# Optimization experiments

Measured on AMD Instinct MI355X. Metric: run time of the kernel, lower is better.

The kernel has to match this reference:

```python
import jax, jax.numpy as jnp
import numpy as np

B, C, H, W = 4, 64, 64, 64  # x shape; mask is (B,1,8H,8W)


def _conv(x, w, pad=0):
    return jax.lax.conv_general_dilated(
        x, w, (1, 1), [(pad, pad), (pad, pad)],
        dimension_numbers=('NCHW', 'OIHW', 'NCHW'))


def _inorm(x, eps=1e-5):  # InstanceNorm2d, affine=False, biased var (torch default)
    mu = x.mean(axis=(2, 3), keepdims=True)
    var = x.var(axis=(2, 3), keepdims=True)
    return (x - mu) * jax.lax.rsqrt(var + eps)


def _forward(x, mask, kconv_w1, kconv_w2, fs_w1, fs_w2, fs_b2, fs_fuse_w):
    b, c, h, w = x.shape
    n = h * w
    # MaxPool2d(8,8) then binarize
    m = jax.lax.reduce_window(mask, -jnp.inf, jax.lax.max,
                              (1, 1, 8, 8), (1, 1, 8, 8), 'VALID')
    m = (m > 0).astype(x.dtype)
    back = 1.0 - m
    # ResidualBlock K_conv (shared for K and Q paths in original code)
    y = jax.nn.relu(_inorm(_conv(x, kconv_w1, pad=1)))
    y = _inorm(_conv(y, kconv_w2, pad=1))
    kx = jax.nn.relu(y + x)
    # L2-normalized K/Q over channel dim
    K = (kx * back).reshape(b, c, n)
    K = K / (jnp.linalg.norm(K, axis=1, keepdims=True) + 1e-8)
    Q = (kx * m).reshape(b, c, n)
    Q = Q / (jnp.linalg.norm(Q, axis=1, keepdims=True) + 1e-8)
    V = (x * back).reshape(b, c, n)
    # cosine-similarity score map, temperature 20
    score = jnp.einsum('bcq,bck->bqk', Q, K) * 20.0  # (b, n_q, n_k)
    qm = m.reshape(b, 1, n)      # query mask (foreground)
    km = back.reshape(b, 1, n)   # key mask (background)
    NEG = -1000000.0
    validx = score + (1.0 - km) * NEG + (1.0 - qm.transpose(0, 2, 1)) * NEG
    att = jax.nn.softmax(validx, axis=-1) * (qm.transpose(0, 2, 1) * km)
    # att_fore[b,c,q] = sum_k V[b,c,k] * att[b,q,k]
    att_fore = jnp.einsum('bck,bqk->bcq', V, att).reshape(b, c, h, w)
    # Fusion_score
    feat1 = _conv(jnp.concatenate([x * m, att_fore * m], axis=1), fs_w1)
    s = jax.nn.sigmoid(_conv(feat1, fs_w2) + fs_b2[None, :, None, None])
    fused = _conv(jnp.concatenate([x * m, att_fore * m * (1.0 - s)], axis=1), fs_fuse_w)
    fs_out = fused * m + x * (1.0 - m)
    out = fs_out * m + x * (1.0 - m)
    # visualization attention mask
    visatt = att.sum(axis=1).reshape(b, 1, h, w)
    attmask = jnp.repeat(jnp.repeat(visatt, 8, axis=2), 8, axis=3)  # nearest upsample x8
    attmask = attmask / attmask.max()
    return out, attmask


def setup_inputs() -> dict:
    key = jax.random.key(0)
    ks = jax.random.split(key, 8)

    def wgt(k, shape, fan_in):
        return jax.random.normal(k, shape, jnp.float32) / np.sqrt(fan_in)

    x = jax.random.normal(ks[0], (B, C, H, W), jnp.float32)
    # sparse foreground mask so maxpool(8x8)>0 yields a mixed fg/bg mask
    mask = (jax.random.uniform(ks[1], (B, 1, H * 8, W * 8)) < 0.01).astype(jnp.float32)
    return dict(
        x=x, mask=mask,
        kconv_w1=wgt(ks[2], (C, C, 3, 3), C * 9),
        kconv_w2=wgt(ks[3], (C, C, 3, 3), C * 9),
        fs_w1=wgt(ks[4], (C, 2 * C, 1, 1), 2 * C),
        fs_w2=wgt(ks[5], (C, C, 1, 1), C),
        fs_b2=jnp.zeros((C,), jnp.float32),
        fs_fuse_w=wgt(ks[6], (C, 2 * C, 1, 1), 2 * C),
    )


def reference(x, mask, kconv_w1, kconv_w2, fs_w1, fs_w2, fs_b2, fs_fuse_w):
    return _forward(x, mask, kconv_w1, kconv_w2, fs_w1, fs_w2, fs_b2, fs_fuse_w)
```

## Files before the change

### kernel.cpp

```cpp
#include <hip/hip_runtime.h>
#include <hip/hip_bf16.h>

typedef __hip_bfloat16 bf16;
typedef __attribute__((ext_vector_type(8))) short short8;
typedef __attribute__((ext_vector_type(4))) float f32x4;
typedef __attribute__((ext_vector_type(16))) float f32x16;

#define BB 4
#define CC 64
#define NN 4096
#define MH 512
#define MW 512
#define LS 72
#define NPARTS 16
#define NDEN 16

#define WB_Y1T  ((size_t)0)
#define WB_VIS  ((size_t)4259840)
#define WB_QIX  ((size_t)4325376)
#define WB_KIX  ((size_t)4390912)
#define WB_MFL  ((size_t)4456448)
#define WB_CNT  ((size_t)4472832)
#define WB_WT1  ((size_t)4476992)
#define WB_WT2  ((size_t)4550720)
#define WB_WFB  ((size_t)4624448)
#define WB_KC   ((size_t)5242880)
#define WB_XT   ((size_t)8388608)
#define WB_KXT  ((size_t)10485760)
#define WB_VT   ((size_t)12582912)
#define WB_QC   ((size_t)14680064)
#define WB_E    ((size_t)16777216)
#define EB_ELEM ((size_t)16777216)
#define WB_AFCP ((size_t)150994944)
#define WB_DENP ((size_t)218103808)
#define WB_VISP ((size_t)220200960)
#define WB_GST  ((size_t)220725248)

__device__ __forceinline__ float us2f(unsigned short u) { return __uint_as_float(((unsigned)u) << 16); }
__device__ __forceinline__ unsigned short f2bu(float f) {
  bf16 h = __float2bfloat16(f);
  return *(unsigned short*)&h;
}

__global__ __launch_bounds__(256) void k_pre(const float* __restrict__ x,
                                             const float* __restrict__ mask,
                                             const float* __restrict__ w1,
                                             const float* __restrict__ w2,
                                             const float* __restrict__ fw1,
                                             const float* __restrict__ fw2,
                                             const float* __restrict__ fwf,
                                             float* __restrict__ outp,
                                             unsigned short* __restrict__ xt,
                                             unsigned char* __restrict__ mfl,
                                             float* __restrict__ vis,
                                             unsigned int* __restrict__ vmaxb,
                                             unsigned short* __restrict__ wT1,
                                             unsigned short* __restrict__ wT2,
                                             unsigned short* __restrict__ wfb) {
  __shared__ float lx[64][65];
  int t = threadIdx.x;
  if (blockIdx.x < 256) {
    int b = blockIdx.x >> 6, p0 = (blockIdx.x & 63) * 64;
    const float* xb = x + (size_t)b * CC * NN + p0;
    float* ob = outp + (size_t)b * CC * NN + p0;
    for (int idx = t; idx < 4096; idx += 256) {
      int c = idx >> 6, j = idx & 63;
      float v = xb[c * NN + j];
      lx[j][c] = v;
      ob[c * NN + j] = v;
    }
    __syncthreads();
    unsigned short* xo = xt + ((size_t)b * NN + p0) * 64;
    for (int idx = t; idx < 2048; idx += 256) {
      int j = idx >> 5, c2 = (idx & 31) * 2;
      ushort2 w2v;
      w2v.x = f2bu(lx[j][c2]);
      w2v.y = f2bu(lx[j][c2 + 1]);
      *(ushort2*)&xo[j * 64 + c2] = w2v;
    }
  } else {
    int g = (blockIdx.x - 256) * 256 + t;
    int o = g >> 2, sub = g & 3;
    int b = o >> 12, p = o & 4095;
    int py = p >> 6, px = p & 63;
    const float* mb = mask + (size_t)b * MH * MW + (py * 8 + sub * 2) * MW + px * 8;
    float mx = 0.f;
    #pragma unroll
    for (int dy = 0; dy < 2; ++dy) {
      const float4* r4 = (const float4*)(mb + dy * MW);
      float4 a = r4[0], c = r4[1];
      mx = fmaxf(mx, fmaxf(fmaxf(a.x, a.y), fmaxf(a.z, a.w)));
      mx = fmaxf(mx, fmaxf(fmaxf(c.x, c.y), fmaxf(c.z, c.w)));
    }
    mx = fmaxf(mx, __shfl_xor(mx, 1));
    mx = fmaxf(mx, __shfl_xor(mx, 2));
    if (sub == 0) {
      mfl[o] = (mx > 0.f) ? 1 : 0;
      vis[o] = 0.f;
    }
    if (g == 0) vmaxb[0] = 0u;
    if (g < 36864) {
      int tap = g >> 12;
      int rem = g & 4095;
      int co = rem >> 6, ci = rem & 63;
      int src = (co * 64 + ci) * 9 + tap;
      wT1[g] = f2bu(w1[src]);
      wT2[g] = f2bu(w2[src]);
    } else if (g < 57344) {
      int j2 = g - 36864;
      if (j2 < 8192)       wfb[j2] = f2bu(fw1[j2]);
      else if (j2 < 12288) wfb[j2] = f2bu(fw2[j2 - 8192]);
      else                 wfb[j2] = f2bu(fwf[j2 - 12288]);
    }
  }
}

__global__ __launch_bounds__(256) void k_compact(const unsigned char* __restrict__ mfl,
                                                 int* __restrict__ qidx, int* __restrict__ kidx,
                                                 int* __restrict__ nq, int* __restrict__ nk) {
  int b = blockIdx.x;
  __shared__ unsigned char lm[4096];
  int t = threadIdx.x;
  *(uint4*)&lm[t * 16] = *(const uint4*)&mfl[b * NN + t * 16];
  __syncthreads();
  if (t >= 64) return;
  int lane = t;
  int qb = 0, kb = 0;
  #pragma unroll
  for (int it = 0; it < 64; ++it) {
    int p = it * 64 + lane;
    bool f = lm[p] != 0;
    unsigned long long bal = __ballot(f);
    int before = __popcll(bal & ((1ULL << lane) - 1ULL));
    if (f)  qidx[b * NN + qb + before] = p;
    if (!f) kidx[b * NN + kb + (lane - before)] = p;
    int cnt = __popcll(bal);
    qb += cnt; kb += 64 - cnt;
  }
  if (lane == 0) { nq[b] = qb; nk[b] = kb; }
}

template <bool NORM_IN>
__global__ __launch_bounds__(256) void k_convm(const unsigned short* __restrict__ src,
                                               const unsigned short* __restrict__ wT,
                                               const float* __restrict__ insum,
                                               const float* __restrict__ insq,
                                               unsigned short* __restrict__ dst,
                                               float* __restrict__ gsump,
                                               float* __restrict__ gsqp) {
  int b = blockIdx.y;
  int r = blockIdx.x;
  __shared__ unsigned short bx[198 * LS];
  __shared__ float nmean[64], ninv[64];
  int t = threadIdx.x;
  if (NORM_IN) {
    if (t < 64) {
      float s = 0.f, s2v = 0.f;
      #pragma unroll 8
      for (int r2 = 0; r2 < 64; ++r2) {
        s   += insum[((size_t)r2 * BB + b) * 64 + t];
        s2v += insq [((size_t)r2 * BB + b) * 64 + t];
      }
      float m = s * (1.f / NN);
      float v = fmaxf(s2v * (1.f / NN) - m * m, 0.f);
      nmean[t] = m; ninv[t] = rsqrtf(v + 1e-5f);
    }
    __syncthreads();
  }
  const unsigned short* sb = src + (size_t)b * NN * 64;
  for (int idx = t; idx < 198 * 8; idx += 256) {
    int row = idx >> 3, c8 = (idx & 7) * 8;
    int dy = row / 66;
    int cx = row - dy * 66 - 1;
    int rr = r + dy - 1;
    uint4 v = make_uint4(0u, 0u, 0u, 0u);
    if ((unsigned)rr < 64u && (unsigned)cx < 64u) {
      v = *(const uint4*)(sb + ((size_t)(rr * 64 + cx)) * 64 + c8);
      if (NORM_IN) {
        unsigned short* e = (unsigned short*)&v;
        #pragma unroll
        for (int j = 0; j < 8; ++j)
          e[j] = f2bu(fmaxf((us2f(e[j]) - nmean[c8 + j]) * ninv[c8 + j], 0.f));
      }
    }
    *(uint4*)&bx[row * LS + c8] = v;
  }
  __syncthreads();
  int lane = t & 63;
  int quad = lane >> 4, col = lane & 15;
  int qw = (t >> 6) * 16;
  f32x4 acc[4] = {{0.f,0.f,0.f,0.f},{0.f,0.f,0.f,0.f},{0.f,0.f,0.f,0.f},{0.f,0.f,0.f,0.f}};
  #pragma unroll
  for (int tap = 0; tap < 9; ++tap) {
    int dy = tap / 3, dx = tap - dy * 3 - 1;
    const unsigned short* wrow = wT + ((size_t)tap * 64 + qw + col) * 64;
    short8 a0 = *(const short8*)(wrow + quad * 8);
    short8 a1 = *(const short8*)(wrow + 32 + quad * 8);
    int rbase = dy * 66 + dx + 1;
    #pragma unroll
    for (int nt = 0; nt < 4; ++nt) {
      int row = rbase + nt * 16 + col;
      short8 b0 = *(const short8*)&bx[row * LS + quad * 8];
      short8 b1 = *(const short8*)&bx[row * LS + 32 + quad * 8];
      acc[nt] = __builtin_amdgcn_mfma_f32_16x16x32_bf16(a0, b0, acc[nt], 0, 0, 0);
      acc[nt] = __builtin_amdgcn_mfma_f32_16x16x32_bf16(a1, b1, acc[nt], 0, 0, 0);
    }
  }
  #pragma unroll
  for (int rr = 0; rr < 4; ++rr) {
    float s1 = acc[0][rr] + acc[1][rr] + acc[2][rr] + acc[3][rr];
    float s2 = acc[0][rr]*acc[0][rr] + acc[1][rr]*acc[1][rr]
             + acc[2][rr]*acc[2][rr] + acc[3][rr]*acc[3][rr];
    s1 += __shfl_xor(s1, 1); s2 += __shfl_xor(s2, 1);
    s1 += __shfl_xor(s1, 2); s2 += __shfl_xor(s2, 2);
    s1 += __shfl_xor(s1, 4); s2 += __shfl_xor(s2, 4);
    s1 += __shfl_xor(s1, 8); s2 += __shfl_xor(s2, 8);
    if (col == 0) {
      int co = qw + quad * 4 + rr;
      gsump[((size_t)r * BB + b) * 64 + co] = s1;
      gsqp [((size_t)r * BB + b) * 64 + co] = s2;
    }
  }
  __syncthreads();
  #pragma unroll
  for (int nt = 0; nt < 4; ++nt)
    #pragma unroll
    for (int rr = 0; rr < 4; ++rr)
      bx[(nt * 16 + col) * LS + qw + quad * 4 + rr] = f2bu(acc[nt][rr]);
  __syncthreads();
  unsigned short* db = dst + ((size_t)b * NN + r * 64) * 64;
  for (int idx = t; idx < 512; idx += 256) {
    int px = idx >> 3, c8 = (idx & 7) * 8;
    *(uint4*)(db + (size_t)px * 64 + c8) = *(const uint4*)&bx[px * LS + c8];
  }
}

__global__ __launch_bounds__(256) void k_gath(const unsigned short* __restrict__ kxt,
                                              const unsigned short* __restrict__ xt,
                                              const int* __restrict__ qidx, const int* __restrict__ kidx,
                                              const int* __restrict__ nqv, const int* __restrict__ nkv,
                                              const float* __restrict__ gsump,
                                              const float* __restrict__ gsqp,
                                              unsigned short* __restrict__ kc,
                                              unsigned short* __restrict__ vt,
                                              unsigned short* __restrict__ qc) {
  int b = blockIdx.y;
  int j0 = blockIdx.x * 64;
  int nqb = nqv[b], nkb = nkv[b];
  int NKP = (nkb + 63) & ~63, NQP = (nqb + 63) & ~63;
  bool dok = j0 < NKP, doq = j0 < NQP;
  if (!dok && !doq) return;
  __shared__ int li[128];
  __shared__ unsigned short tv[64 * LS];
  __shared__ float m2[64], i2[64];
  int t = threadIdx.x;
  if (t < 64) li[t] = (j0 + t < nkb) ? kidx[b * NN + j0 + t] : -1;
  if (t >= 64 && t < 128) li[t] = (j0 + (t - 64) < nqb) ? qidx[b * NN + j0 + (t - 64)] : -1;
  if (t >= 128 && t < 192) {
    int c = t - 128;
    float s = 0.f, s2v = 0.f;
    #pragma unroll 8
    for (int r2 = 0; r2 < 64; ++r2) {
      s   += gsump[((size_t)r2 * BB + b) * 64 + c];
      s2v += gsqp [((size_t)r2 * BB + b) * 64 + c];
    }
    float m = s * (1.f / NN);
    float v = fmaxf(s2v * (1.f / NN) - m * m, 0.f);
    m2[c] = m; i2[c] = rsqrtf(v + 1e-5f);
  }
  __syncthreads();
  const unsigned short* kxb = kxt + (size_t)b * NN * 64;
  const unsigned short* xtb = xt + (size_t)b * NN * 64;
  uint4 z = make_uint4(0u, 0u, 0u, 0u);
  for (int idx = t; idx < 512; idx += 256) {
    int row = idx >> 3, c8 = (idx & 7) * 8;
    size_t dsto = ((size_t)b * NN + j0 + row) * 64 + c8;
    if (dok) {
      int sk = li[row];
      uint4 ko = z;
      if (sk >= 0) {
        uint4 kv = *(const uint4*)(kxb + (size_t)sk * 64 + c8);
        uint4 xv = *(const uint4*)(xtb + (size_t)sk * 64 + c8);
        const unsigned short* ke = (const unsigned short*)&kv;
        const unsigned short* xe = (const unsigned short*)&xv;
        float f[8]; float ss = 0.f;
        #pragma unroll
        for (int j = 0; j < 8; ++j) {
          float v = fmaxf((us2f(ke[j]) - m2[c8 + j]) * i2[c8 + j] + us2f(xe[j]), 0.f);
          f[j] = v; ss += v * v;
        }
        ss += __shfl_xor(ss, 1); ss += __shfl_xor(ss, 2); ss += __shfl_xor(ss, 4);
        float inv = 1.f / (sqrtf(ss) + 1e-8f);
        unsigned short* oe = (unsigned short*)&ko;
        #pragma unroll
        for (int j = 0; j < 8; ++j) oe[j] = f2bu(f[j] * inv);
        *(uint4*)&tv[row * LS + c8] = xv;
      } else {
        float ss = 0.f;
        ss += __shfl_xor(ss, 1); ss += __shfl_xor(ss, 2); ss += __shfl_xor(ss, 4);
        *(uint4*)&tv[row * LS + c8] = z;
      }
      *(uint4*)(kc + dsto) = ko;
    }
    if (doq) {
      int sq = li[64 + row];
      uint4 qo = z;
      if (sq >= 0) {
        uint4 kv = *(const uint4*)(kxb + (size_t)sq * 64 + c8);
        uint4 xv = *(const uint4*)(xtb + (size_t)sq * 64 + c8);
        const unsigned short* ke = (const unsigned short*)&kv;
        const unsigned short* xe = (const unsigned short*)&xv;
        float f[8]; float ss = 0.f;
        #pragma unroll
        for (int j = 0; j < 8; ++j) {
          float v = fmaxf((us2f(ke[j]) - m2[c8 + j]) * i2[c8 + j] + us2f(xe[j]), 0.f);
          f[j] = v; ss += v * v;
        }
        ss += __shfl_xor(ss, 1); ss += __shfl_xor(ss, 2); ss += __shfl_xor(ss, 4);
        float inv = 1.f / (sqrtf(ss) + 1e-8f);
        unsigned short* oe = (unsigned short*)&qo;
        #pragma unroll
        for (int j = 0; j < 8; ++j) oe[j] = f2bu(f[j] * inv);
      } else {
        float ss = 0.f;
        ss += __shfl_xor(ss, 1); ss += __shfl_xor(ss, 2); ss += __shfl_xor(ss, 4);
      }
      *(uint4*)(qc + dsto) = qo;
    }
  }
  __syncthreads();
  if (!dok) return;
  for (int idx = t; idx < 512; idx += 256) {
    int c = idx >> 3, k8 = (idx & 7) * 8;
    unsigned short vals[8];
    #pragma unroll
    for (int j = 0; j < 8; ++j) vals[j] = tv[(k8 + j) * LS + c];
    *(uint4*)(vt + (size_t)b * 262144 + (size_t)c * 4096 + j0 + k8) = *(const uint4*)&vals[0];
  }
}

__global__ __launch_bounds__(256) void k_att1(const unsigned short* __restrict__ kc,
                                              const unsigned short* __restrict__ vt,
                                              const unsigned short* __restrict__ qc,
                                              const int* __restrict__ nqv, const int* __restrict__ nkv,
                                              unsigned short* __restrict__ afc_part,
                                              float* __restrict__ den_part,
                                              unsigned short* __restrict__ eg) {
  __shared__ unsigned short leb[4][32 * LS];
  int b = blockIdx.y;
  int nqb = nqv[b], nkb = nkv[b];
  int t = threadIdx.x;
  int wave = t >> 6, lane = t & 63;
  int part = blockIdx.x & (NPARTS - 1);
  int q0 = ((blockIdx.x >> 4) * 4 + wave) * 32;
  if (q0 >= nqb) return;
  int ntiles = (nkb + 63) >> 6;
  int nt_blk = (part < ntiles) ? ((ntiles - part + NPARTS - 1) >> 4) : 0;
  int NKP = (nkb + 63) & ~63;
  unsigned short* le = leb[wave];
  int l31 = lane & 31, lhi = lane >> 5;
  const unsigned short* kcb = kc + (size_t)b * NN * 64;
  const unsigned short* vtb = vt + (size_t)b * 262144;
  const unsigned short* qcb = qc + (size_t)b * NN * 64;
  unsigned short* egb = eg + (size_t)b * EB_ELEM;
  unsigned short* afcp = afc_part + ((size_t)b * NN) * (NPARTS * 64);
  float* denp = den_part + ((size_t)b * NN) * NDEN;
  short8 aq[4];
  #pragma unroll
  for (int ks = 0; ks < 4; ++ks)
    aq[ks] = *(const short8*)(qcb + (size_t)(q0 + l31) * 64 + ks * 16 + lhi * 8);
  f32x16 pv0, pv1, dsum;
  #pragma unroll
  for (int i = 0; i < 16; ++i) { pv0[i] = 0.f; pv1[i] = 0.f; dsum[i] = 0.f; }
  for (int it = 0; it < nt_blk; ++it) {
    int j0 = (part + it * NPARTS) * 64;
    #pragma unroll
    for (int kh = 0; kh < 2; ++kh) {
      f32x16 s;
      #pragma unroll
      for (int i = 0; i < 16; ++i) s[i] = 0.f;
      const unsigned short* krow = kcb + (size_t)(j0 + kh * 32 + l31) * 64 + lhi * 8;
      #pragma unroll
      for (int ks = 0; ks < 4; ++ks) {
        short8 bk = *(const short8*)(krow + ks * 16);
        s = __builtin_amdgcn_mfma_f32_32x32x16_bf16(aq[ks], bk, s, 0, 0, 0);
      }
      bool kval = (j0 + kh * 32 + l31) < nkb;
      #pragma unroll
      for (int reg = 0; reg < 16; ++reg) {
        float e = kval ? __expf(20.f * s[reg]) : 0.f;
        dsum[reg] += e;
        int row = (reg & 3) + 8 * (reg >> 2) + 4 * lhi;
        le[row * LS + kh * 32 + l31] = f2bu(e);
      }
    }
    #pragma unroll
    for (int ks = 0; ks < 4; ++ks) {
      short8 a = *(const short8*)&le[l31 * LS + ks * 16 + lhi * 8];
      short8 bv0 = *(const short8*)(vtb + (size_t)l31 * 4096 + j0 + ks * 16 + lhi * 8);
      short8 bv1 = *(const short8*)(vtb + (size_t)(32 + l31) * 4096 + j0 + ks * 16 + lhi * 8);
      pv0 = __builtin_amdgcn_mfma_f32_32x32x16_bf16(a, bv0, pv0, 0, 0, 0);
      pv1 = __builtin_amdgcn_mfma_f32_32x32x16_bf16(a, bv1, pv1, 0, 0, 0);
    }
    #pragma unroll
    for (int sub = 0; sub < 4; ++sub) {
      int idx = sub * 64 + lane;
      int q = idx >> 3, cc8 = (idx & 7) * 8;
      if (q0 + q < nqb)
        *(uint4*)(egb + (size_t)(q0 + q) * NKP + j0 + cc8) = *(const uint4*)&le[q * LS + cc8];
    }
  }
  #pragma unroll
  for (int reg = 0; reg < 16; ++reg) {
    float v = dsum[reg];
    v += __shfl_xor(v, 1); v += __shfl_xor(v, 2); v += __shfl_xor(v, 4);
    v += __shfl_xor(v, 8); v += __shfl_xor(v, 16);
    int row = (reg & 3) + 8 * (reg >> 2) + 4 * lhi;
    int qq = q0 + row;
    if (l31 == 0 && qq < nqb) denp[(size_t)qq * NDEN + part] = v;
  }
  #pragma unroll
  for (int reg = 0; reg < 16; ++reg) {
    int row = (reg & 3) + 8 * (reg >> 2) + 4 * lhi;
    int qq = q0 + row;
    if (qq < nqb) {
      unsigned short* ap = afcp + ((size_t)qq * NPARTS + part) * 64;
      ap[l31]      = f2bu(pv0[reg]);
      ap[32 + l31] = f2bu(pv1[reg]);
    }
  }
}

__global__ __launch_bounds__(256) void k_vis(const unsigned short* __restrict__ eg,
                                             const float* __restrict__ den_part,
                                             const int* __restrict__ nqv, const int* __restrict__ nkv,
                                             float* __restrict__ visp) {
  int b = blockIdx.z;
  int nqb = nqv[b], nkb = nkv[b];
  int k0 = blockIdx.x * 256;
  if (k0 >= nkb) return;
  int NKP = (nkb + 63) & ~63;
  int qpart = blockIdx.y;
  int qbeg = (qpart * nqb) >> 3;
  int qend = ((qpart + 1) * nqb) >> 3;
  __shared__ float wd[256];
  int t = threadIdx.x;
  int k = k0 + t;
  const unsigned short* eb = eg + (size_t)b * EB_ELEM;
  float acc = 0.f;
  for (int qc = qbeg; qc < qend; qc += 256) {
    __syncthreads();
    int qq = qc + t;
    float d = 0.f;
    if (qq < qend) {
      const float4* dp = (const float4*)(den_part + ((size_t)b * NN + qq) * NDEN);
      float4 a0 = dp[0], a1 = dp[1], a2 = dp[2], a3 = dp[3];
      d = ((a0.x + a0.y) + (a0.z + a0.w)) + ((a1.x + a1.y) + (a1.z + a1.w))
        + ((a2.x + a2.y) + (a2.z + a2.w)) + ((a3.x + a3.y) + (a3.z + a3.w));
    }
    wd[t] = (d > 0.f) ? 1.f / d : 0.f;
    __syncthreads();
    int lim = min(256, qend - qc);
    if (k < nkb) {
      const unsigned short* ep = eb + (size_t)qc * NKP + k;
      int j = 0;
      for (; j + 8 <= lim; j += 8) {
        #pragma unroll
        for (int u = 0; u < 8; ++u)
          acc += us2f(ep[(size_t)(j + u) * NKP]) * wd[j + u];
      }
      for (; j < lim; ++j)
        acc += us2f(ep[(size_t)j * NKP]) * wd[j];
    }
  }
  if (k < nkb) visp[((size_t)qpart * BB + b) * NN + k] = acc;
}

#define FS 136
__global__ __launch_bounds__(256) void k_fusionm(const unsigned short* __restrict__ xt,
                                                 const unsigned short* __restrict__ afc_part,
                                                 const float* __restrict__ den_part,
                                                 const int* __restrict__ qidx, const int* __restrict__ nqv,
                                                 const unsigned short* __restrict__ wall,
                                                 const float* __restrict__ b2,
                                                 float* __restrict__ outp) {
  int b = blockIdx.y;
  int nqb = nqv[b];
  int q0 = blockIdx.x * 64;
  if (q0 >= nqb) return;
  __shared__ unsigned short pxa[64 * FS];
  __shared__ unsigned short f1s[64 * LS];
  __shared__ int qpl[64];
  int t = threadIdx.x;
  int lane = t & 63;
  int quad = lane >> 4, col = lane & 15;
  int cb = (t >> 6) * 16;
  const int* qix = qidx + b * NN;
  const unsigned short* xtb = xt + (size_t)b * NN * 64;
  const unsigned short* w1b = wall;
  const unsigned short* w2b = wall + 8192;
  const unsigned short* wfb = wall + 12288;
  short8 a1[4], a2[2], af[4];
  #pragma unroll
  for (int kt = 0; kt < 4; ++kt) {
    a1[kt] = *(const short8*)&w1b[(cb + col) * 128 + kt * 32 + quad * 8];
    af[kt] = *(const short8*)&wfb[(cb + col) * 128 + kt * 32 + quad * 8];
  }
  #pragma unroll
  for (int kt = 0; kt < 2; ++kt)
    a2[kt] = *(const short8*)&w2b[(cb + col) * 64 + kt * 32 + quad * 8];
  float b2v[4];
  #pragma unroll
  for (int r = 0; r < 4; ++r) b2v[r] = b2[cb + quad * 4 + r];
  if (t < 64) qpl[t] = (q0 + t < nqb) ? qix[q0 + t] : -1;
  for (int idx = t; idx < 512; idx += 256) {
    int q = idx >> 3, c8 = (idx & 7) * 8;
    int qq = q0 + q;
    uint4 pv = make_uint4(0u, 0u, 0u, 0u);
    unsigned short pa8[8] = {0, 0, 0, 0, 0, 0, 0, 0};
    if (qq < nqb) {
      int qp = qix[qq];
      pv = *(const uint4*)(xtb + (size_t)qp * 64 + c8);
      const float* db = den_part + ((size_t)b * NN + qq) * NDEN;
      float d = 0.f;
      #pragma unroll
      for (int p2 = 0; p2 < NDEN; ++p2) d += db[p2];
      float av[8];
      #pragma unroll
      for (int j = 0; j < 8; ++j) av[j] = 0.f;
      const unsigned short* ab = afc_part + ((size_t)b * NN + qq) * (NPARTS * 64) + c8;
      #pragma unroll
      for (int p2 = 0; p2 < NPARTS; ++p2) {
        const uint4 u = *(const uint4*)(ab + p2 * 64);
        const unsigned short* e8 = (const unsigned short*)&u;
        #pragma unroll
        for (int j = 0; j < 8; ++j) av[j] += us2f(e8[j]);
      }
      float invd = (d > 0.f) ? 1.f / d : 0.f;
      #pragma unroll
      for (int j = 0; j < 8; ++j) pa8[j] = f2bu(av[j] * invd);
    }
    *(uint4*)&pxa[q * FS + c8] = pv;
    *(uint4*)&pxa[q * FS + 64 + c8] = *(const uint4*)&pa8[0];
  }
  __syncthreads();
  #pragma unroll
  for (int qt = 0; qt < 4; ++qt) {
    f32x4 acc = {0.f, 0.f, 0.f, 0.f};
    #pragma unroll
    for (int kt = 0; kt < 4; ++kt) {
      short8 bfrag = *(const short8*)&pxa[(qt * 16 + col) * FS + kt * 32 + quad * 8];
      acc = __builtin_amdgcn_mfma_f32_16x16x32_bf16(a1[kt], bfrag, acc, 0, 0, 0);
    }
    #pragma unroll
    for (int r = 0; r < 4; ++r)
      f1s[(qt * 16 + col) * LS + cb + quad * 4 + r] = f2bu(acc[r]);
  }
  __syncthreads();
  #pragma unroll
  for (int qt = 0; qt < 4; ++qt) {
    f32x4 acc = {0.f, 0.f, 0.f, 0.f};
    #pragma unroll
    for (int kt = 0; kt < 2; ++kt) {
      short8 bfrag = *(const short8*)&f1s[(qt * 16 + col) * LS + kt * 32 + quad * 8];
      acc = __builtin_amdgcn_mfma_f32_16x16x32_bf16(a2[kt], bfrag, acc, 0, 0, 0);
    }
    #pragma unroll
    for (int r = 0; r < 4; ++r) {
      float sg = 1.f / (1.f + __expf(-(acc[r] + b2v[r])));
      int addr = (qt * 16 + col) * FS + 64 + cb + quad * 4 + r;
      pxa[addr] = f2bu(us2f(pxa[addr]) * (1.f - sg));
    }
  }
  __syncthreads();
  #pragma unroll
  for (int qt = 0; qt < 4; ++qt) {
    f32x4 acc = {0.f, 0.f, 0.f, 0.f};
    #pragma unroll
    for (int kt = 0; kt < 4; ++kt) {
      short8 bfrag = *(const short8*)&pxa[(qt * 16 + col) * FS + kt * 32 + quad * 8];
      acc = __builtin_amdgcn_mfma_f32_16x16x32_bf16(af[kt], bfrag, acc, 0, 0, 0);
    }
    int qp = qpl[qt * 16 + col];
    if (qp >= 0) {
      #pragma unroll
      for (int r = 0; r < 4; ++r)
        outp[((size_t)b * CC + cb + quad * 4 + r) * NN + qp] = acc[r];
    }
  }
}

__global__ __launch_bounds__(256) void k_vmax(const float* __restrict__ visp,
                                              const int* __restrict__ kidx,
                                              const int* __restrict__ nkv,
                                              float* __restrict__ vis,
                                              unsigned int* __restrict__ vmaxb) {
  int i = blockIdx.x * 256 + threadIdx.x;
  int b = i >> 12, k = i & 4095;
  float v = 0.f;
  if (k < nkv[b]) {
    #pragma unroll
    for (int p2 = 0; p2 < 8; ++p2) v += visp[((size_t)p2 * BB + b) * NN + k];
    vis[b * NN + kidx[b * NN + k]] = v;
  }
  #pragma unroll
  for (int off = 32; off > 0; off >>= 1) v = fmaxf(v, __shfl_down(v, off));
  if ((threadIdx.x & 63) == 0) atomicMax(vmaxb, __float_as_uint(v));
}

__global__ __launch_bounds__(256) void k_upsample(const float* __restrict__ vis,
                                                  const unsigned int* __restrict__ vmaxb,
                                                  float* __restrict__ out2) {
  int i4 = blockIdx.x * 256 + threadIdx.x;
  int b = i4 >> 16;
  int rem = i4 & 65535;
  int y = rem >> 7, x4 = (rem & 127) * 4;
  float vm = __uint_as_float(vmaxb[0]);
  if (!(vm > 0.f)) vm = 1.f;
  float v = vis[b * NN + (y >> 3) * 64 + (x4 >> 3)] / vm;
  ((float4*)out2)[i4] = make_float4(v, v, v, v);
}

extern "C" void kernel_launch(void* const* d_in, const int* in_sizes, int n_in,
                              void* d_out, int out_size, void* d_ws, size_t ws_size,
                              hipStream_t stream) {
  const float* x    = (const float*)d_in[0];
  const float* mask = (const float*)d_in[1];
  const float* w1   = (const float*)d_in[2];
  const float* w2c  = (const float*)d_in[3];
  const float* fsw1 = (const float*)d_in[4];
  const float* fsw2 = (const float*)d_in[5];
  const float* fsb2 = (const float*)d_in[6];
  const float* fswf = (const float*)d_in[7];
  float* out = (float*)d_out;
  char* wsb = (char*)d_ws;

  float* vis = (float*)(wsb + WB_VIS);
  int* qidx  = (int*)(wsb + WB_QIX);
  int* kidx  = (int*)(wsb + WB_KIX);
  unsigned char* mfl = (unsigned char*)(wsb + WB_MFL);
  int* nq = (int*)(wsb + WB_CNT);
  int* nk = nq + 4;
  unsigned int* vmaxb = (unsigned int*)(nq + 8);
  unsigned short* wT1 = (unsigned short*)(wsb + WB_WT1);
  unsigned short* wT2 = (unsigned short*)(wsb + WB_WT2);
  unsigned short* wall = (unsigned short*)(wsb + WB_WFB);
  unsigned short* y1t = (unsigned short*)(wsb + WB_Y1T);
  unsigned short* xt  = (unsigned short*)(wsb + WB_XT);
  unsigned short* kxt = (unsigned short*)(wsb + WB_KXT);
  unsigned short* kc  = (unsigned short*)(wsb + WB_KC);
  unsigned short* vt  = (unsigned short*)(wsb + WB_VT);
  unsigned short* qc  = (unsigned short*)(wsb + WB_QC);
  unsigned short* eg  = (unsigned short*)(wsb + WB_E);
  unsigned short* afc_part = (unsigned short*)(wsb + WB_AFCP);
  float* den_part = (float*)(wsb + WB_DENP);
  float* visp     = (float*)(wsb + WB_VISP);
  float* gsum1p = (float*)(wsb + WB_GST);
  float* gsq1p  = (float*)(wsb + WB_GST + 65536);
  float* gsum2p = (float*)(wsb + WB_GST + 131072);
  float* gsq2p  = (float*)(wsb + WB_GST + 196608);

  k_pre<<<512, 256, 0, stream>>>(x, mask, w1, w2c, fsw1, fsw2, fswf,
                                 out, xt, mfl, vis, vmaxb, wT1, wT2, wall);
  k_compact<<<4, 256, 0, stream>>>(mfl, qidx, kidx, nq, nk);
  k_convm<false><<<dim3(64, BB), 256, 0, stream>>>(xt, wT1, nullptr, nullptr, y1t, gsum1p, gsq1p);
  k_convm<true><<<dim3(64, BB), 256, 0, stream>>>(y1t, wT2, gsum1p, gsq1p, kxt, gsum2p, gsq2p);
  k_gath<<<dim3(64, BB), 256, 0, stream>>>(kxt, xt, qidx, kidx, nq, nk, gsum2p, gsq2p, kc, vt, qc);
  k_att1<<<dim3(32 * NPARTS, BB), 256, 0, stream>>>(kc, vt, qc, nq, nk, afc_part, den_part, eg);
  k_vis<<<dim3(16, 8, BB), 256, 0, stream>>>(eg, den_part, nq, nk, visp);
  k_fusionm<<<dim3(64, BB), 256, 0, stream>>>(xt, afc_part, den_part, qidx, nq, wall, fsb2, out);
  k_vmax<<<64, 256, 0, stream>>>(visp, kidx, nk, vis, vmaxb);
  k_upsample<<<1024, 256, 0, stream>>>(vis, vmaxb, out + 1048576);
}
```

Measured before the change: 174.0 us.

## Fuse all stages into one cooperative persistent kernel with grid-wide syncs

Replaces the ten separate kernel launches with a single cooperative kernel. It loops grid-stride over the former per-stage block indices and separates the stages with grid.sync(). This removes per-launch overhead and the idle gaps between small kernels. In exchange, every grid barrier stalls the whole GPU, occupancy is capped by the largest shared-memory and register footprint of any stage, and the grid size comes from an occupancy query.

```diff
diff --git a/kernel.cpp b/kernel.cpp
--- a/kernel.cpp
+++ b/kernel.cpp
@@ -1,5 +1,8 @@
 #include <hip/hip_runtime.h>
 #include <hip/hip_bf16.h>
+#include <hip/hip_cooperative_groups.h>
+
+namespace cg = cooperative_groups;
 
 typedef __hip_bfloat16 bf16;
 typedef __attribute__((ext_vector_type(8))) short short8;
@@ -14,6 +17,7 @@
 #define LS 72
 #define NPARTS 16
 #define NDEN 16
+#define FS 136
 
 #define WB_Y1T  ((size_t)0)
 #define WB_VIS  ((size_t)4259840)
@@ -42,132 +46,14 @@
   return *(unsigned short*)&h;
 }
 
-__global__ __launch_bounds__(256) void k_pre(const float* __restrict__ x,
-                                             const float* __restrict__ mask,
-                                             const float* __restrict__ w1,
-                                             const float* __restrict__ w2,
-                                             const float* __restrict__ fw1,
-                                             const float* __restrict__ fw2,
-                                             const float* __restrict__ fwf,
-                                             float* __restrict__ outp,
-                                             unsigned short* __restrict__ xt,
-                                             unsigned char* __restrict__ mfl,
-                                             float* __restrict__ vis,
-                                             unsigned int* __restrict__ vmaxb,
-                                             unsigned short* __restrict__ wT1,
-                                             unsigned short* __restrict__ wT2,
-                                             unsigned short* __restrict__ wfb) {
-  __shared__ float lx[64][65];
-  int t = threadIdx.x;
-  if (blockIdx.x < 256) {
-    int b = blockIdx.x >> 6, p0 = (blockIdx.x & 63) * 64;
-    const float* xb = x + (size_t)b * CC * NN + p0;
-    float* ob = outp + (size_t)b * CC * NN + p0;
-    for (int idx = t; idx < 4096; idx += 256) {
-      int c = idx >> 6, j = idx & 63;
-      float v = xb[c * NN + j];
-      lx[j][c] = v;
-      ob[c * NN + j] = v;
-    }
-    __syncthreads();
-    unsigned short* xo = xt + ((size_t)b * NN + p0) * 64;
-    for (int idx = t; idx < 2048; idx += 256) {
-      int j = idx >> 5, c2 = (idx & 31) * 2;
-      ushort2 w2v;
-      w2v.x = f2bu(lx[j][c2]);
-      w2v.y = f2bu(lx[j][c2 + 1]);
-      *(ushort2*)&xo[j * 64 + c2] = w2v;
-    }
-  } else {
-    int g = (blockIdx.x - 256) * 256 + t;
-    int o = g >> 2, sub = g & 3;
-    int b = o >> 12, p = o & 4095;
-    int py = p >> 6, px = p & 63;
-    const float* mb = mask + (size_t)b * MH * MW + (py * 8 + sub * 2) * MW + px * 8;
-    float mx = 0.f;
-    #pragma unroll
-    for (int dy = 0; dy < 2; ++dy) {
-      const float4* r4 = (const float4*)(mb + dy * MW);
-      float4 a = r4[0], c = r4[1];
-      mx = fmaxf(mx, fmaxf(fmaxf(a.x, a.y), fmaxf(a.z, a.w)));
-      mx = fmaxf(mx, fmaxf(fmaxf(c.x, c.y), fmaxf(c.z, c.w)));
-    }
-    mx = fmaxf(mx, __shfl_xor(mx, 1));
-    mx = fmaxf(mx, __shfl_xor(mx, 2));
-    if (sub == 0) {
-      mfl[o] = (mx > 0.f) ? 1 : 0;
-      vis[o] = 0.f;
-    }
-    if (g == 0) vmaxb[0] = 0u;
-    if (g < 36864) {
-      int tap = g >> 12;
-      int rem = g & 4095;
-      int co = rem >> 6, ci = rem & 63;
-      int src = (co * 64 + ci) * 9 + tap;
-      wT1[g] = f2bu(w1[src]);
-      wT2[g] = f2bu(w2[src]);
-    } else if (g < 57344) {
-      int j2 = g - 36864;
-      if (j2 < 8192)       wfb[j2] = f2bu(fw1[j2]);
-      else if (j2 < 12288) wfb[j2] = f2bu(fw2[j2 - 8192]);
-      else                 wfb[j2] = f2bu(fwf[j2 - 12288]);
-    }
-  }
-}
-
-__global__ __launch_bounds__(256) void k_compact(const unsigned char* __restrict__ mfl,
-                                                 int* __restrict__ qidx, int* __restrict__ kidx,
-                                                 int* __restrict__ nq, int* __restrict__ nk) {
-  int b = blockIdx.x;
-  __shared__ unsigned char lm[4096];
-  int t = threadIdx.x;
-  *(uint4*)&lm[t * 16] = *(const uint4*)&mfl[b * NN + t * 16];
-  __syncthreads();
-  if (t >= 64) return;
-  int lane = t;
-  int qb = 0, kb = 0;
-  #pragma unroll
-  for (int it = 0; it < 64; ++it) {
-    int p = it * 64 + lane;
-    bool f = lm[p] != 0;
-    unsigned long long bal = __ballot(f);
-    int before = __popcll(bal & ((1ULL << lane) - 1ULL));
-    if (f)  qidx[b * NN + qb + before] = p;
-    if (!f) kidx[b * NN + kb + (lane - before)] = p;
-    int cnt = __popcll(bal);
-    qb += cnt; kb += 64 - cnt;
-  }
-  if (lane == 0) { nq[b] = qb; nk[b] = kb; }
-}
-
-template <bool NORM_IN>
-__global__ __launch_bounds__(256) void k_convm(const unsigned short* __restrict__ src,
-                                               const unsigned short* __restrict__ wT,
-                                               const float* __restrict__ insum,
-                                               const float* __restrict__ insq,
-                                               unsigned short* __restrict__ dst,
-                                               float* __restrict__ gsump,
-                                               float* __restrict__ gsqp) {
-  int b = blockIdx.y;
-  int r = blockIdx.x;
-  __shared__ unsigned short bx[198 * LS];
-  __shared__ float nmean[64], ninv[64];
-  int t = threadIdx.x;
-  if (NORM_IN) {
-    if (t < 64) {
-      float s = 0.f, s2v = 0.f;
-      #pragma unroll 8
-      for (int r2 = 0; r2 < 64; ++r2) {
-        s   += insum[((size_t)r2 * BB + b) * 64 + t];
-        s2v += insq [((size_t)r2 * BB + b) * 64 + t];
-      }
-      float m = s * (1.f / NN);
-      float v = fmaxf(s2v * (1.f / NN) - m * m, 0.f);
-      nmean[t] = m; ninv[t] = rsqrtf(v + 1e-5f);
-    }
-    __syncthreads();
-  }
-  const unsigned short* sb = src + (size_t)b * NN * 64;
+__device__ __forceinline__ void conv_body(const unsigned short* __restrict__ sb,
+                                          const unsigned short* __restrict__ wT,
+                                          unsigned short* __restrict__ db,
+                                          float* __restrict__ gsump,
+                                          float* __restrict__ gsqp,
+                                          unsigned short* bxs,
+                                          const float* nmean, const float* ninv,
+                                          bool norm_in, int r, int b, int t) {
   for (int idx = t; idx < 198 * 8; idx += 256) {
     int row = idx >> 3, c8 = (idx & 7) * 8;
     int dy = row / 66;
@@ -176,14 +62,14 @@
     uint4 v = make_uint4(0u, 0u, 0u, 0u);
     if ((unsigned)rr < 64u && (unsigned)cx < 64u) {
       v = *(const uint4*)(sb + ((size_t)(rr * 64 + cx)) * 64 + c8);
-      if (NORM_IN) {
+      if (norm_in) {
         unsigned short* e = (unsigned short*)&v;
         #pragma unroll
         for (int j = 0; j < 8; ++j)
           e[j] = f2bu(fmaxf((us2f(e[j]) - nmean[c8 + j]) * ninv[c8 + j], 0.f));
       }
     }
-    *(uint4*)&bx[row * LS + c8] = v;
+    *(uint4*)&bxs[row * LS + c8] = v;
   }
   __syncthreads();
   int lane = t & 63;
@@ -200,8 +86,8 @@
     #pragma unroll
     for (int nt = 0; nt < 4; ++nt) {
       int row = rbase + nt * 16 + col;
-      short8 b0 = *(const short8*)&bx[row * LS + quad * 8];
-      short8 b1 = *(const short8*)&bx[row * LS + 32 + quad * 8];
+      short8 b0 = *(const short8*)&bxs[row * LS + quad * 8];
+      short8 b1 = *(const short8*)&bxs[row * LS + 32 + quad * 8];
       acc[nt] = __builtin_amdgcn_mfma_f32_16x16x32_bf16(a0, b0, acc[nt], 0, 0, 0);
       acc[nt] = __builtin_amdgcn_mfma_f32_16x16x32_bf16(a1, b1, acc[nt], 0, 0, 0);
     }
@@ -226,422 +112,35 @@
   for (int nt = 0; nt < 4; ++nt)
     #pragma unroll
     for (int rr = 0; rr < 4; ++rr)
-      bx[(nt * 16 + col) * LS + qw + quad * 4 + rr] = f2bu(acc[nt][rr]);
+      bxs[(nt * 16 + col) * LS + qw + quad * 4 + rr] = f2bu(acc[nt][rr]);
   __syncthreads();
-  unsigned short* db = dst + ((size_t)b * NN + r * 64) * 64;
   for (int idx = t; idx < 512; idx += 256) {
     int px = idx >> 3, c8 = (idx & 7) * 8;
-    *(uint4*)(db + (size_t)px * 64 + c8) = *(const uint4*)&bx[px * LS + c8];
+    *(uint4*)(db + (size_t)px * 64 + c8) = *(const uint4*)&bxs[px * LS + c8];
   }
 }
 
-__global__ __launch_bounds__(256) void k_gath(const unsigned short* __restrict__ kxt,
-                                              const unsigned short* __restrict__ xt,
-                                              const int* __restrict__ qidx, const int* __restrict__ kidx,
-                                              const int* __restrict__ nqv, const int* __restrict__ nkv,
-                                              const float* __restrict__ gsump,
-                                              const float* __restrict__ gsqp,
-                                              unsigned short* __restrict__ kc,
-                                              unsigned short* __restrict__ vt,
-                                              unsigned short* __restrict__ qc) {
-  int b = blockIdx.y;
-  int j0 = blockIdx.x * 64;
-  int nqb = nqv[b], nkb = nkv[b];
-  int NKP = (nkb + 63) & ~63, NQP = (nqb + 63) & ~63;
-  bool dok = j0 < NKP, doq = j0 < NQP;
-  if (!dok && !doq) return;
-  __shared__ int li[128];
-  __shared__ unsigned short tv[64 * LS];
-  __shared__ float m2[64], i2[64];
+__global__ __launch_bounds__(256, 2) void k_mega(const float* __restrict__ x,
+                                                 const float* __restrict__ mask,
+                                                 const float* __restrict__ w1g,
+                                                 const float* __restrict__ w2g,
+                                                 const float* __restrict__ fw1,
+                                                 const float* __restrict__ fw2,
+                                                 const float* __restrict__ fb2,
+                                                 const float* __restrict__ fwf,
+                                                 float* __restrict__ outp,
+                                                 char* __restrict__ wsb) {
+  __shared__ __align__(16) char smem[29056];
+  cg::grid_group grid = cg::this_grid();
   int t = threadIdx.x;
-  if (t < 64) li[t] = (j0 + t < nkb) ? kidx[b * NN + j0 + t] : -1;
-  if (t >= 64 && t < 128) li[t] = (j0 + (t - 64) < nqb) ? qidx[b * NN + j0 + (t - 64)] : -1;
-  if (t >= 128 && t < 192) {
-    int c = t - 128;
-    float s = 0.f, s2v = 0.f;
-    #pragma unroll 8
-    for (int r2 = 0; r2 < 64; ++r2) {
-      s   += gsump[((size_t)r2 * BB + b) * 64 + c];
-      s2v += gsqp [((size_t)r2 * BB + b) * 64 + c];
-    }
-    float m = s * (1.f / NN);
-    float v = fmaxf(s2v * (1.f / NN) - m * m, 0.f);
-    m2[c] = m; i2[c] = rsqrtf(v + 1e-5f);
-  }
-  __syncthreads();
-  const unsigned short* kxb = kxt + (size_t)b * NN * 64;
-  const unsigned short* xtb = xt + (size_t)b * NN * 64;
-  uint4 z = make_uint4(0u, 0u, 0u, 0u);
-  for (int idx = t; idx < 512; idx += 256) {
-    int row = idx >> 3, c8 = (idx & 7) * 8;
-    size_t dsto = ((size_t)b * NN + j0 + row) * 64 + c8;
-    if (dok) {
-      int sk = li[row];
-      uint4 ko = z;
-      if (sk >= 0) {
-        uint4 kv = *(const uint4*)(kxb + (size_t)sk * 64 + c8);
-        uint4 xv = *(const uint4*)(xtb + (size_t)sk * 64 + c8);
-        const unsigned short* ke = (const unsigned short*)&kv;
-        const unsigned short* xe = (const unsigned short*)&xv;
-        float f[8]; float ss = 0.f;
-        #pragma unroll
-        for (int j = 0; j < 8; ++j) {
-          float v = fmaxf((us2f(ke[j]) - m2[c8 + j]) * i2[c8 + j] + us2f(xe[j]), 0.f);
-          f[j] = v; ss += v * v;
-        }
-        ss += __shfl_xor(ss, 1); ss += __shfl_xor(ss, 2); ss += __shfl_xor(ss, 4);
-        float inv = 1.f / (sqrtf(ss) + 1e-8f);
-        unsigned short* oe = (unsigned short*)&ko;
-        #pragma unroll
-        for (int j = 0; j < 8; ++j) oe[j] = f2bu(f[j] * inv);
-        *(uint4*)&tv[row * LS + c8] = xv;
-      } else {
-        float ss = 0.f;
-        ss += __shfl_xor(ss, 1); ss += __shfl_xor(ss, 2); ss += __shfl_xor(ss, 4);
-        *(uint4*)&tv[row * LS + c8] = z;
-      }
-      *(uint4*)(kc + dsto) = ko;
-    }
-    if (doq) {
-      int sq = li[64 + row];
-      uint4 qo = z;
-      if (sq >= 0) {
-        uint4 kv = *(const uint4*)(kxb + (size_t)sq * 64 + c8);
-        uint4 xv = *(const uint4*)(xtb + (size_t)sq * 64 + c8);
-        const unsigned short* ke = (const unsigned short*)&kv;
-        const unsigned short* xe = (const unsigned short*)&xv;
-        float f[8]; float ss = 0.f;
-        #pragma unroll
-        for (int j = 0; j < 8; ++j) {
-          float v = fmaxf((us2f(ke[j]) - m2[c8 + j]) * i2[c8 + j] + us2f(xe[j]), 0.f);
-          f[j] = v; ss += v * v;
-        }
-        ss += __shfl_xor(ss, 1); ss += __shfl_xor(ss, 2); ss += __shfl_xor(ss, 4);
-        float inv = 1.f / (sqrtf(ss) + 1e-8f);
-        unsigned short* oe = (unsigned short*)&qo;
-        #pragma unroll
-        for (int j = 0; j < 8; ++j) oe[j] = f2bu(f[j] * inv);
-      } else {
-        float ss = 0.f;
-        ss += __shfl_xor(ss, 1); ss += __shfl_xor(ss, 2); ss += __shfl_xor(ss, 4);
-      }
-      *(uint4*)(qc + dsto) = qo;
-    }
-  }
-  __syncthreads();
-  if (!dok) return;
-  for (int idx = t; idx < 512; idx += 256) {
-    int c = idx >> 3, k8 = (idx & 7) * 8;
-    unsigned short vals[8];
-    #pragma unroll
-    for (int j = 0; j < 8; ++j) vals[j] = tv[(k8 + j) * LS + c];
-    *(uint4*)(vt + (size_t)b * 262144 + (size_t)c * 4096 + j0 + k8) = *(const uint4*)&vals[0];
-  }
-}
-
-__global__ __launch_bounds__(256) void k_att1(const unsigned short* __restrict__ kc,
-                                              const unsigned short* __restrict__ vt,
-                                              const unsigned short* __restrict__ qc,
-                                              const int* __restrict__ nqv, const int* __restrict__ nkv,
-                                              unsigned short* __restrict__ afc_part,
-                                              float* __restrict__ den_part,
-                                              unsigned short* __restrict__ eg) {
-  __shared__ unsigned short leb[4][32 * LS];
-  int b = blockIdx.y;
-  int nqb = nqv[b], nkb = nkv[b];
-  int t = threadIdx.x;
-  int wave = t >> 6, lane = t & 63;
-  int part = blockIdx.x & (NPARTS - 1);
-  int q0 = ((blockIdx.x >> 4) * 4 + wave) * 32;
-  if (q0 >= nqb) return;
-  int ntiles = (nkb + 63) >> 6;
-  int nt_blk = (part < ntiles) ? ((ntiles - part + NPARTS - 1) >> 4) : 0;
-  int NKP = (nkb + 63) & ~63;
-  unsigned short* le = leb[wave];
-  int l31 = lane & 31, lhi = lane >> 5;
-  const unsigned short* kcb = kc + (size_t)b * NN * 64;
-  const unsigned short* vtb = vt + (size_t)b * 262144;
-  const unsigned short* qcb = qc + (size_t)b * NN * 64;
-  unsigned short* egb = eg + (size_t)b * EB_ELEM;
-  unsigned short* afcp = afc_part + ((size_t)b * NN) * (NPARTS * 64);
-  float* denp = den_part + ((size_t)b * NN) * NDEN;
-  short8 aq[4];
-  #pragma unroll
-  for (int ks = 0; ks < 4; ++ks)
-    aq[ks] = *(const short8*)(qcb + (size_t)(q0 + l31) * 64 + ks * 16 + lhi * 8);
-  f32x16 pv0, pv1, dsum;
-  #pragma unroll
-  for (int i = 0; i < 16; ++i) { pv0[i] = 0.f; pv1[i] = 0.f; dsum[i] = 0.f; }
-  for (int it = 0; it < nt_blk; ++it) {
-    int j0 = (part + it * NPARTS) * 64;
-    #pragma unroll
-    for (int kh = 0; kh < 2; ++kh) {
-      f32x16 s;
-      #pragma unroll
-      for (int i = 0; i < 16; ++i) s[i] = 0.f;
-      const unsigned short* krow = kcb + (size_t)(j0 + kh * 32 + l31) * 64 + lhi * 8;
-      #pragma unroll
-      for (int ks = 0; ks < 4; ++ks) {
-        short8 bk = *(const short8*)(krow + ks * 16);
-        s = __builtin_amdgcn_mfma_f32_32x32x16_bf16(aq[ks], bk, s, 0, 0, 0);
-      }
-      bool kval = (j0 + kh * 32 + l31) < nkb;
-      #pragma unroll
-      for (int reg = 0; reg < 16; ++reg) {
-        float e = kval ? __expf(20.f * s[reg]) : 0.f;
-        dsum[reg] += e;
-        int row = (reg & 3) + 8 * (reg >> 2) + 4 * lhi;
-        le[row * LS + kh * 32 + l31] = f2bu(e);
-      }
-    }
-    #pragma unroll
-    for (int ks = 0; ks < 4; ++ks) {
-      short8 a = *(const short8*)&le[l31 * LS + ks * 16 + lhi * 8];
-      short8 bv0 = *(const short8*)(vtb + (size_t)l31 * 4096 + j0 + ks * 16 + lhi * 8);
-      short8 bv1 = *(const short8*)(vtb + (size_t)(32 + l31) * 4096 + j0 + ks * 16 + lhi * 8);
-      pv0 = __builtin_amdgcn_mfma_f32_32x32x16_bf16(a, bv0, pv0, 0, 0, 0);
-      pv1 = __builtin_amdgcn_mfma_f32_32x32x16_bf16(a, bv1, pv1, 0, 0, 0);
-    }
-    #pragma unroll
-    for (int sub = 0; sub < 4; ++sub) {
-      int idx = sub * 64 + lane;
-      int q = idx >> 3, cc8 = (idx & 7) * 8;
-      if (q0 + q < nqb)
-        *(uint4*)(egb + (size_t)(q0 + q) * NKP + j0 + cc8) = *(const uint4*)&le[q * LS + cc8];
-    }
-  }
-  #pragma unroll
-  for (int reg = 0; reg < 16; ++reg) {
-    float v = dsum[reg];
-    v += __shfl_xor(v, 1); v += __shfl_xor(v, 2); v += __shfl_xor(v, 4);
-    v += __shfl_xor(v, 8); v += __shfl_xor(v, 16);
-    int row = (reg & 3) + 8 * (reg >> 2) + 4 * lhi;
-    int qq = q0 + row;
-    if (l31 == 0 && qq < nqb) denp[(size_t)qq * NDEN + part] = v;
-  }
-  #pragma unroll
-  for (int reg = 0; reg < 16; ++reg) {
-    int row = (reg & 3) + 8 * (reg >> 2) + 4 * lhi;
-    int qq = q0 + row;
-    if (qq < nqb) {
-      unsigned short* ap = afcp + ((size_t)qq * NPARTS + part) * 64;
-      ap[l31]      = f2bu(pv0[reg]);
-      ap[32 + l31] = f2bu(pv1[reg]);
-    }
-  }
-}
-
-__global__ __launch_bounds__(256) void k_vis(const unsigned short* __restrict__ eg,
-                                             const float* __restrict__ den_part,
-                                             const int* __restrict__ nqv, const int* __restrict__ nkv,
-                                             float* __restrict__ visp) {
-  int b = blockIdx.z;
-  int nqb = nqv[b], nkb = nkv[b];
-  int k0 = blockIdx.x * 256;
-  if (k0 >= nkb) return;
-  int NKP = (nkb + 63) & ~63;
-  int qpart = blockIdx.y;
-  int qbeg = (qpart * nqb) >> 3;
-  int qend = ((qpart + 1) * nqb) >> 3;
-  __shared__ float wd[256];
-  int t = threadIdx.x;
-  int k = k0 + t;
-  const unsigned short* eb = eg + (size_t)b * EB_ELEM;
-  float acc = 0.f;
-  for (int qc = qbeg; qc < qend; qc += 256) {
-    __syncthreads();
-    int qq = qc + t;
-    float d = 0.f;
-    if (qq < qend) {
-      const float4* dp = (const float4*)(den_part + ((size_t)b * NN + qq) * NDEN);
-      float4 a0 = dp[0], a1 = dp[1], a2 = dp[2], a3 = dp[3];
-      d = ((a0.x + a0.y) + (a0.z + a0.w)) + ((a1.x + a1.y) + (a1.z + a1.w))
-        + ((a2.x + a2.y) + (a2.z + a2.w)) + ((a3.x + a3.y) + (a3.z + a3.w));
-    }
-    wd[t] = (d > 0.f) ? 1.f / d : 0.f;
-    __syncthreads();
-    int lim = min(256, qend - qc);
-    if (k < nkb) {
-      const unsigned short* ep = eb + (size_t)qc * NKP + k;
-      int j = 0;
-      for (; j + 8 <= lim; j += 8) {
-        #pragma unroll
-        for (int u = 0; u < 8; ++u)
-          acc += us2f(ep[(size_t)(j + u) * NKP]) * wd[j + u];
-      }
-      for (; j < lim; ++j)
-        acc += us2f(ep[(size_t)j * NKP]) * wd[j];
-    }
-  }
-  if (k < nkb) visp[((size_t)qpart * BB + b) * NN + k] = acc;
-}
-
-#define FS 136
-__global__ __launch_bounds__(256) void k_fusionm(const unsigned short* __restrict__ xt,
-                                                 const unsigned short* __restrict__ afc_part,
-                                                 const float* __restrict__ den_part,
-                                                 const int* __restrict__ qidx, const int* __restrict__ nqv,
-                                                 const unsigned short* __restrict__ wall,
-                                                 const float* __restrict__ b2,
-                                                 float* __restrict__ outp) {
-  int b = blockIdx.y;
-  int nqb = nqv[b];
-  int q0 = blockIdx.x * 64;
-  if (q0 >= nqb) return;
-  __shared__ unsigned short pxa[64 * FS];
-  __shared__ unsigned short f1s[64 * LS];
-  __shared__ int qpl[64];
-  int t = threadIdx.x;
-  int lane = t & 63;
-  int quad = lane >> 4, col = lane & 15;
-  int cb = (t >> 6) * 16;
-  const int* qix = qidx + b * NN;
-  const unsigned short* xtb = xt + (size_t)b * NN * 64;
-  const unsigned short* w1b = wall;
-  const unsigned short* w2b = wall + 8192;
-  const unsigned short* wfb = wall + 12288;
-  short8 a1[4], a2[2], af[4];
-  #pragma unroll
-  for (int kt = 0; kt < 4; ++kt) {
-    a1[kt] = *(const short8*)&w1b[(cb + col) * 128 + kt * 32 + quad * 8];
-    af[kt] = *(const short8*)&wfb[(cb + col) * 128 + kt * 32 + quad * 8];
-  }
-  #pragma unroll
-  for (int kt = 0; kt < 2; ++kt)
-    a2[kt] = *(const short8*)&w2b[(cb + col) * 64 + kt * 32 + quad * 8];
-  float b2v[4];
-  #pragma unroll
-  for (int r = 0; r < 4; ++r) b2v[r] = b2[cb + quad * 4 + r];
-  if (t < 64) qpl[t] = (q0 + t < nqb) ? qix[q0 + t] : -1;
-  for (int idx = t; idx < 512; idx += 256) {
-    int q = idx >> 3, c8 = (idx & 7) * 8;
-    int qq = q0 + q;
-    uint4 pv = make_uint4(0u, 0u, 0u, 0u);
-    unsigned short pa8[8] = {0, 0, 0, 0, 0, 0, 0, 0};
-    if (qq < nqb) {
-      int qp = qix[qq];
-      pv = *(const uint4*)(xtb + (size_t)qp * 64 + c8);
-      const float* db = den_part + ((size_t)b * NN + qq) * NDEN;
-      float d = 0.f;
-      #pragma unroll
-      for (int p2 = 0; p2 < NDEN; ++p2) d += db[p2];
-      float av[8];
-      #pragma unroll
-      for (int j = 0; j < 8; ++j) av[j] = 0.f;
-      const unsigned short* ab = afc_part + ((size_t)b * NN + qq) * (NPARTS * 64) + c8;
-      #pragma unroll
-      for (int p2 = 0; p2 < NPARTS; ++p2) {
-        const uint4 u = *(const uint4*)(ab + p2 * 64);
-        const unsigned short* e8 = (const unsigned short*)&u;
-        #pragma unroll
-        for (int j = 0; j < 8; ++j) av[j] += us2f(e8[j]);
-      }
-      float invd = (d > 0.f) ? 1.f / d : 0.f;
-      #pragma unroll
-      for (int j = 0; j < 8; ++j) pa8[j] = f2bu(av[j] * invd);
-    }
-    *(uint4*)&pxa[q * FS + c8] = pv;
-    *(uint4*)&pxa[q * FS + 64 + c8] = *(const uint4*)&pa8[0];
-  }
-  __syncthreads();
-  #pragma unroll
-  for (int qt = 0; qt < 4; ++qt) {
-    f32x4 acc = {0.f, 0.f, 0.f, 0.f};
-    #pragma unroll
-    for (int kt = 0; kt < 4; ++kt) {
-      short8 bfrag = *(const short8*)&pxa[(qt * 16 + col) * FS + kt * 32 + quad * 8];
-      acc = __builtin_amdgcn_mfma_f32_16x16x32_bf16(a1[kt], bfrag, acc, 0, 0, 0);
-    }
-    #pragma unroll
-    for (int r = 0; r < 4; ++r)
-      f1s[(qt * 16 + col) * LS + cb + quad * 4 + r] = f2bu(acc[r]);
-  }
-  __syncthreads();
-  #pragma unroll
-  for (int qt = 0; qt < 4; ++qt) {
-    f32x4 acc = {0.f, 0.f, 0.f, 0.f};
-    #pragma unroll
-    for (int kt = 0; kt < 2; ++kt) {
-      short8 bfrag = *(const short8*)&f1s[(qt * 16 + col) * LS + kt * 32 + quad * 8];
-      acc = __builtin_amdgcn_mfma_f32_16x16x32_bf16(a2[kt], bfrag, acc, 0, 0, 0);
-    }
-    #pragma unroll
-    for (int r = 0; r < 4; ++r) {
-      float sg = 1.f / (1.f + __expf(-(acc[r] + b2v[r])));
-      int addr = (qt * 16 + col) * FS + 64 + cb + quad * 4 + r;
-      pxa[addr] = f2bu(us2f(pxa[addr]) * (1.f - sg));
-    }
-  }
-  __syncthreads();
-  #pragma unroll
-  for (int qt = 0; qt < 4; ++qt) {
-    f32x4 acc = {0.f, 0.f, 0.f, 0.f};
-    #pragma unroll
-    for (int kt = 0; kt < 4; ++kt) {
-      short8 bfrag = *(const short8*)&pxa[(qt * 16 + col) * FS + kt * 32 + quad * 8];
-      acc = __builtin_amdgcn_mfma_f32_16x16x32_bf16(af[kt], bfrag, acc, 0, 0, 0);
-    }
-    int qp = qpl[qt * 16 + col];
-    if (qp >= 0) {
-      #pragma unroll
-      for (int r = 0; r < 4; ++r)
-        outp[((size_t)b * CC + cb + quad * 4 + r) * NN + qp] = acc[r];
-    }
-  }
-}
-
-__global__ __launch_bounds__(256) void k_vmax(const float* __restrict__ visp,
-                                              const int* __restrict__ kidx,
-                                              const int* __restrict__ nkv,
-                                              float* __restrict__ vis,
-                                              unsigned int* __restrict__ vmaxb) {
-  int i = blockIdx.x * 256 + threadIdx.x;
-  int b = i >> 12, k = i & 4095;
-  float v = 0.f;
-  if (k < nkv[b]) {
-    #pragma unroll
-    for (int p2 = 0; p2 < 8; ++p2) v += visp[((size_t)p2 * BB + b) * NN + k];
-    vis[b * NN + kidx[b * NN + k]] = v;
-  }
-  #pragma unroll
-  for (int off = 32; off > 0; off >>= 1) v = fmaxf(v, __shfl_down(v, off));
-  if ((threadIdx.x & 63) == 0) atomicMax(vmaxb, __float_as_uint(v));
-}
-
-__global__ __launch_bounds__(256) void k_upsample(const float* __restrict__ vis,
-                                                  const unsigned int* __restrict__ vmaxb,
-                                                  float* __restrict__ out2) {
-  int i4 = blockIdx.x * 256 + threadIdx.x;
-  int b = i4 >> 16;
-  int rem = i4 & 65535;
-  int y = rem >> 7, x4 = (rem & 127) * 4;
-  float vm = __uint_as_float(vmaxb[0]);
-  if (!(vm > 0.f)) vm = 1.f;
-  float v = vis[b * NN + (y >> 3) * 64 + (x4 >> 3)] / vm;
-  ((float4*)out2)[i4] = make_float4(v, v, v, v);
-}
-
-extern "C" void kernel_launch(void* const* d_in, const int* in_sizes, int n_in,
-                              void* d_out, int out_size, void* d_ws, size_t ws_size,
-                              hipStream_t stream) {
-  const float* x    = (const float*)d_in[0];
-  const float* mask = (const float*)d_in[1];
-  const float* w1   = (const float*)d_in[2];
-  const float* w2c  = (const float*)d_in[3];
-  const float* fsw1 = (const float*)d_in[4];
-  const float* fsw2 = (const float*)d_in[5];
-  const float* fsb2 = (const float*)d_in[6];
-  const float* fswf = (const float*)d_in[7];
-  float* out = (float*)d_out;
-  char* wsb = (char*)d_ws;
 
   float* vis = (float*)(wsb + WB_VIS);
   int* qidx  = (int*)(wsb + WB_QIX);
   int* kidx  = (int*)(wsb + WB_KIX);
   unsigned char* mfl = (unsigned char*)(wsb + WB_MFL);
-  int* nq = (int*)(wsb + WB_CNT);
-  int* nk = nq + 4;
-  unsigned int* vmaxb = (unsigned int*)(nq + 8);
+  int* nqv = (int*)(wsb + WB_CNT);
+  int* nkv = nqv + 4;
+  unsigned int* vmaxb = (unsigned int*)(nqv + 8);
   unsigned short* wT1 = (unsigned short*)(wsb + WB_WT1);
   unsigned short* wT2 = (unsigned short*)(wsb + WB_WT2);
   unsigned short* wall = (unsigned short*)(wsb + WB_WFB);
@@ -659,16 +158,508 @@
   float* gsq1p  = (float*)(wsb + WB_GST + 65536);
   float* gsum2p = (float*)(wsb + WB_GST + 131072);
   float* gsq2p  = (float*)(wsb + WB_GST + 196608);
-
-  k_pre<<<512, 256, 0, stream>>>(x, mask, w1, w2c, fsw1, fsw2, fswf,
-                                 out, xt, mfl, vis, vmaxb, wT1, wT2, wall);
-  k_compact<<<4, 256, 0, stream>>>(mfl, qidx, kidx, nq, nk);
-  k_convm<false><<<dim3(64, BB), 256, 0, stream>>>(xt, wT1, nullptr, nullptr, y1t, gsum1p, gsq1p);
-  k_convm<true><<<dim3(64, BB), 256, 0, stream>>>(y1t, wT2, gsum1p, gsq1p, kxt, gsum2p, gsq2p);
-  k_gath<<<dim3(64, BB), 256, 0, stream>>>(kxt, xt, qidx, kidx, nq, nk, gsum2p, gsq2p, kc, vt, qc);
-  k_att1<<<dim3(32 * NPARTS, BB), 256, 0, stream>>>(kc, vt, qc, nq, nk, afc_part, den_part, eg);
-  k_vis<<<dim3(16, 8, BB), 256, 0, stream>>>(eg, den_part, nq, nk, visp);
-  k_fusionm<<<dim3(64, BB), 256, 0, stream>>>(xt, afc_part, den_part, qidx, nq, wall, fsb2, out);
-  k_vmax<<<64, 256, 0, stream>>>(visp, kidx, nk, vis, vmaxb);
-  k_upsample<<<1024, 256, 0, stream>>>(vis, vmaxb, out + 1048576);
+  float* out2 = outp + 1048576;
+
+  for (int vb = blockIdx.x; vb < 512; vb += gridDim.x) {
+    __syncthreads();
+    if (vb < 256) {
+      float* lx = (float*)smem;
+      int b = vb >> 6, p0 = (vb & 63) * 64;
+      const float* xb = x + (size_t)b * CC * NN + p0;
+      float* ob = outp + (size_t)b * CC * NN + p0;
+      for (int idx = t; idx < 4096; idx += 256) {
+        int c = idx >> 6, j = idx & 63;
+        float v = xb[c * NN + j];
+        lx[j * 65 + c] = v;
+        ob[c * NN + j] = v;
+      }
+      __syncthreads();
+      unsigned short* xo = xt + ((size_t)b * NN + p0) * 64;
+      for (int idx = t; idx < 2048; idx += 256) {
+        int j = idx >> 5, c2 = (idx & 31) * 2;
+        ushort2 w2v;
+        w2v.x = f2bu(lx[j * 65 + c2]);
+        w2v.y = f2bu(lx[j * 65 + c2 + 1]);
+        *(ushort2*)&xo[j * 64 + c2] = w2v;
+      }
+    } else {
+      int g = (vb - 256) * 256 + t;
+      int o = g >> 2, sub = g & 3;
+      int b = o >> 12, p = o & 4095;
+      int py = p >> 6, px = p & 63;
+      const float* mb = mask + (size_t)b * MH * MW + (py * 8 + sub * 2) * MW + px * 8;
+      float mx = 0.f;
+      #pragma unroll
+      for (int dy = 0; dy < 2; ++dy) {
+        const float4* r4 = (const float4*)(mb + dy * MW);
+        float4 a = r4[0], c = r4[1];
+        mx = fmaxf(mx, fmaxf(fmaxf(a.x, a.y), fmaxf(a.z, a.w)));
+        mx = fmaxf(mx, fmaxf(fmaxf(c.x, c.y), fmaxf(c.z, c.w)));
+      }
+      mx = fmaxf(mx, __shfl_xor(mx, 1));
+      mx = fmaxf(mx, __shfl_xor(mx, 2));
+      if (sub == 0) {
+        mfl[o] = (mx > 0.f) ? 1 : 0;
+        vis[o] = 0.f;
+      }
+      if (g == 0) vmaxb[0] = 0u;
+      if (g < 36864) {
+        int tap = g >> 12;
+        int rem = g & 4095;
+        int co = rem >> 6, ci = rem & 63;
+        int src = (co * 64 + ci) * 9 + tap;
+        wT1[g] = f2bu(w1g[src]);
+        wT2[g] = f2bu(w2g[src]);
+      } else if (g < 57344) {
+        int j2 = g - 36864;
+        if (j2 < 8192)       wall[j2] = f2bu(fw1[j2]);
+        else if (j2 < 12288) wall[j2] = f2bu(fw2[j2 - 8192]);
+        else                 wall[j2] = f2bu(fwf[j2 - 12288]);
+      }
+    }
+  }
+  grid.sync();
+
+  for (int vb = blockIdx.x; vb < 260; vb += gridDim.x) {
+    __syncthreads();
+    int b = vb / 65;
+    int xx = vb - b * 65;
+    if (xx == 64) {
+      unsigned char* lm = (unsigned char*)smem;
+      *(uint4*)&lm[t * 16] = *(const uint4*)&mfl[b * NN + t * 16];
+      __syncthreads();
+      if (t < 64) {
+        int lane = t;
+        int qb = 0, kb = 0;
+        #pragma unroll
+        for (int it = 0; it < 64; ++it) {
+          int p = it * 64 + lane;
+          bool f = lm[p] != 0;
+          unsigned long long bal = __ballot(f);
+          int before = __popcll(bal & ((1ULL << lane) - 1ULL));
+          if (f)  qidx[b * NN + qb + before] = p;
+          if (!f) kidx[b * NN + kb + (lane - before)] = p;
+          int cnt = __popcll(bal);
+          qb += cnt; kb += 64 - cnt;
+        }
+        if (lane == 0) { nqv[b] = qb; nkv[b] = kb; }
+      }
+    } else {
+      conv_body(xt + (size_t)b * NN * 64, wT1, y1t + ((size_t)b * NN + xx * 64) * 64,
+                gsum1p, gsq1p, (unsigned short*)smem, nullptr, nullptr, false, xx, b, t);
+    }
+  }
+  grid.sync();
+
+  for (int vb = blockIdx.x; vb < 256; vb += gridDim.x) {
+    __syncthreads();
+    int b = vb >> 6, r = vb & 63;
+    float* nmean = (float*)(smem + 28512);
+    float* ninv  = nmean + 64;
+    if (t < 64) {
+      float s = 0.f, s2v = 0.f;
+      #pragma unroll 8
+      for (int r2 = 0; r2 < 64; ++r2) {
+        s   += gsum1p[((size_t)r2 * BB + b) * 64 + t];
+        s2v += gsq1p [((size_t)r2 * BB + b) * 64 + t];
+      }
+      float m = s * (1.f / NN);
+      float v = fmaxf(s2v * (1.f / NN) - m * m, 0.f);
+      nmean[t] = m; ninv[t] = rsqrtf(v + 1e-5f);
+    }
+    __syncthreads();
+    conv_body(y1t + (size_t)b * NN * 64, wT2, kxt + ((size_t)b * NN + r * 64) * 64,
+              gsum2p, gsq2p, (unsigned short*)smem, nmean, ninv, true, r, b, t);
+  }
+  grid.sync();
+
+  for (int vb = blockIdx.x; vb < 256; vb += gridDim.x) {
+    __syncthreads();
+    int b = vb >> 6;
+    int j0 = (vb & 63) * 64;
+    int nqb = nqv[b], nkb = nkv[b];
+    int NKP = (nkb + 63) & ~63, NQP = (nqb + 63) & ~63;
+    bool dok = j0 < NKP, doq = j0 < NQP;
+    if (dok || doq) {
+      int* li = (int*)smem;
+      unsigned short* tv = (unsigned short*)(smem + 512);
+      float* m2 = (float*)(smem + 9728);
+      float* i2 = m2 + 64;
+      if (t < 64) li[t] = (j0 + t < nkb) ? kidx[b * NN + j0 + t] : -1;
+      if (t >= 64 && t < 128) li[t] = (j0 + (t - 64) < nqb) ? qidx[b * NN + j0 + (t - 64)] : -1;
+      if (t >= 128 && t < 192) {
+        int c = t - 128;
+        float s = 0.f, s2v = 0.f;
+        #pragma unroll 8
+        for (int r2 = 0; r2 < 64; ++r2) {
+          s   += gsum2p[((size_t)r2 * BB + b) * 64 + c];
+          s2v += gsq2p [((size_t)r2 * BB + b) * 64 + c];
+        }
+        float m = s * (1.f / NN);
+        float v = fmaxf(s2v * (1.f / NN) - m * m, 0.f);
+        m2[c] = m; i2[c] = rsqrtf(v + 1e-5f);
+      }
+      __syncthreads();
+      const unsigned short* kxb = kxt + (size_t)b * NN * 64;
+      const unsigned short* xtb = xt + (size_t)b * NN * 64;
+      uint4 z = make_uint4(0u, 0u, 0u, 0u);
+      for (int idx = t; idx < 512; idx += 256) {
+        int row = idx >> 3, c8 = (idx & 7) * 8;
+        size_t dsto = ((size_t)b * NN + j0 + row) * 64 + c8;
+        if (dok) {
+          int sk = li[row];
+          uint4 ko = z;
+          if (sk >= 0) {
+            uint4 kv = *(const uint4*)(kxb + (size_t)sk * 64 + c8);
+            uint4 xv = *(const uint4*)(xtb + (size_t)sk * 64 + c8);
+            const unsigned short* ke = (const unsigned short*)&kv;
+            const unsigned short* xe = (const unsigned short*)&xv;
+            float f[8]; float ss = 0.f;
+            #pragma unroll
+            for (int j = 0; j < 8; ++j) {
+              float v = fmaxf((us2f(ke[j]) - m2[c8 + j]) * i2[c8 + j] + us2f(xe[j]), 0.f);
+              f[j] = v; ss += v * v;
+            }
+            ss += __shfl_xor(ss, 1); ss += __shfl_xor(ss, 2); ss += __shfl_xor(ss, 4);
+            float inv = 1.f / (sqrtf(ss) + 1e-8f);
+            unsigned short* oe = (unsigned short*)&ko;
+            #pragma unroll
+            for (int j = 0; j < 8; ++j) oe[j] = f2bu(f[j] * inv);
+            *(uint4*)&tv[row * LS + c8] = xv;
+          } else {
+            float ss = 0.f;
+            ss += __shfl_xor(ss, 1); ss += __shfl_xor(ss, 2); ss += __shfl_xor(ss, 4);
+            *(uint4*)&tv[row * LS + c8] = z;
+          }
+          *(uint4*)(kc + dsto) = ko;
+        }
+        if (doq) {
+          int sq = li[64 + row];
+          uint4 qo = z;
+          if (sq >= 0) {
+            uint4 kv = *(const uint4*)(kxb + (size_t)sq * 64 + c8);
+            uint4 xv = *(const uint4*)(xtb + (size_t)sq * 64 + c8);
+            const unsigned short* ke = (const unsigned short*)&kv;
+            const unsigned short* xe = (const unsigned short*)&xv;
+            float f[8]; float ss = 0.f;
+            #pragma unroll
+            for (int j = 0; j < 8; ++j) {
+              float v = fmaxf((us2f(ke[j]) - m2[c8 + j]) * i2[c8 + j] + us2f(xe[j]), 0.f);
+              f[j] = v; ss += v * v;
+            }
+            ss += __shfl_xor(ss, 1); ss += __shfl_xor(ss, 2); ss += __shfl_xor(ss, 4);
+            float inv = 1.f / (sqrtf(ss) + 1e-8f);
+            unsigned short* oe = (unsigned short*)&qo;
+            #pragma unroll
+            for (int j = 0; j < 8; ++j) oe[j] = f2bu(f[j] * inv);
+          } else {
+            float ss = 0.f;
+            ss += __shfl_xor(ss, 1); ss += __shfl_xor(ss, 2); ss += __shfl_xor(ss, 4);
+          }
+          *(uint4*)(qc + dsto) = qo;
+        }
+      }
+      __syncthreads();
+      if (dok) {
+        for (int idx = t; idx < 512; idx += 256) {
+          int c = idx >> 3, k8 = (idx & 7) * 8;
+          unsigned short vals[8];
+          #pragma unroll
+          for (int j = 0; j < 8; ++j) vals[j] = tv[(k8 + j) * LS + c];
+          *(uint4*)(vt + (size_t)b * 262144 + (size_t)c * 4096 + j0 + k8) = *(const uint4*)&vals[0];
+        }
+      }
+    }
+  }
+  grid.sync();
+
+  for (int vb = blockIdx.x; vb < 512 * BB; vb += gridDim.x) {
+    int b = vb >> 9;
+    int xx = vb & 511;
+    int wave = t >> 6, lane = t & 63;
+    int part = xx & (NPARTS - 1);
+    int q0 = ((xx >> 4) * 4 + wave) * 32;
+    int nqb = nqv[b], nkb = nkv[b];
+    if (q0 < nqb) {
+      int ntiles = (nkb + 63) >> 6;
+      int nt_blk = (part < ntiles) ? ((ntiles - part + NPARTS - 1) >> 4) : 0;
+      int NKP = (nkb + 63) & ~63;
+      unsigned short* le = (unsigned short*)smem + wave * (32 * LS);
+      int l31 = lane & 31, lhi = lane >> 5;
+      const unsigned short* kcb = kc + (size_t)b * NN * 64;
+      const unsigned short* vtb = vt + (size_t)b * 262144;
+      const unsigned short* qcb = qc + (size_t)b * NN * 64;
+      unsigned short* egb = eg + (size_t)b * EB_ELEM;
+      unsigned short* afcp = afc_part + ((size_t)b * NN) * (NPARTS * 64);
+      float* denp = den_part + ((size_t)b * NN) * NDEN;
+      short8 aq[4];
+      #pragma unroll
+      for (int ks = 0; ks < 4; ++ks)
+        aq[ks] = *(const short8*)(qcb + (size_t)(q0 + l31) * 64 + ks * 16 + lhi * 8);
+      f32x16 pv0, pv1, dsum;
+      #pragma unroll
+      for (int i = 0; i < 16; ++i) { pv0[i] = 0.f; pv1[i] = 0.f; dsum[i] = 0.f; }
+      for (int it = 0; it < nt_blk; ++it) {
+        int j0 = (part + it * NPARTS) * 64;
+        #pragma unroll
+        for (int kh = 0; kh < 2; ++kh) {
+          f32x16 s;
+          #pragma unroll
+          for (int i = 0; i < 16; ++i) s[i] = 0.f;
+          const unsigned short* krow = kcb + (size_t)(j0 + kh * 32 + l31) * 64 + lhi * 8;
+          #pragma unroll
+          for (int ks = 0; ks < 4; ++ks) {
+            short8 bk = *(const short8*)(krow + ks * 16);
+            s = __builtin_amdgcn_mfma_f32_32x32x16_bf16(aq[ks], bk, s, 0, 0, 0);
+          }
+          bool kval = (j0 + kh * 32 + l31) < nkb;
+          #pragma unroll
+          for (int reg = 0; reg < 16; ++reg) {
+            float e = kval ? __expf(20.f * s[reg]) : 0.f;
+            dsum[reg] += e;
+            int row = (reg & 3) + 8 * (reg >> 2) + 4 * lhi;
+            le[row * LS + kh * 32 + l31] = f2bu(e);
+          }
+        }
+        #pragma unroll
+        for (int ks = 0; ks < 4; ++ks) {
+          short8 a = *(const short8*)&le[l31 * LS + ks * 16 + lhi * 8];
+          short8 bv0 = *(const short8*)(vtb + (size_t)l31 * 4096 + j0 + ks * 16 + lhi * 8);
+          short8 bv1 = *(const short8*)(vtb + (size_t)(32 + l31) * 4096 + j0 + ks * 16 + lhi * 8);
+          pv0 = __builtin_amdgcn_mfma_f32_32x32x16_bf16(a, bv0, pv0, 0, 0, 0);
+          pv1 = __builtin_amdgcn_mfma_f32_32x32x16_bf16(a, bv1, pv1, 0, 0, 0);
+        }
+        #pragma unroll
+        for (int sub = 0; sub < 4; ++sub) {
+          int idx = sub * 64 + lane;
+          int q = idx >> 3, cc8 = (idx & 7) * 8;
+          if (q0 + q < nqb)
+            *(uint4*)(egb + (size_t)(q0 + q) * NKP + j0 + cc8) = *(const uint4*)&le[q * LS + cc8];
+        }
+      }
+      #pragma unroll
+      for (int reg = 0; reg < 16; ++reg) {
+        float v = dsum[reg];
+        v += __shfl_xor(v, 1); v += __shfl_xor(v, 2); v += __shfl_xor(v, 4);
+        v += __shfl_xor(v, 8); v += __shfl_xor(v, 16);
+        int row = (reg & 3) + 8 * (reg >> 2) + 4 * lhi;
+        int qq = q0 + row;
+        if (l31 == 0 && qq < nqb) denp[(size_t)qq * NDEN + part] = v;
+      }
+      #pragma unroll
+      for (int reg = 0; reg < 16; ++reg) {
+        int row = (reg & 3) + 8 * (reg >> 2) + 4 * lhi;
+        int qq = q0 + row;
+        if (qq < nqb) {
+          unsigned short* ap = afcp + ((size_t)qq * NPARTS + part) * 64;
+          ap[l31]      = f2bu(pv0[reg]);
+          ap[32 + l31] = f2bu(pv1[reg]);
+        }
+      }
+    }
+  }
+  grid.sync();
+
+  for (int vb = blockIdx.x; vb < 192 * BB; vb += gridDim.x) {
+    __syncthreads();
+    int b = vb / 192;
+    int xx = vb - b * 192;
+    int nqb = nqv[b], nkb = nkv[b];
+    if (xx < 128) {
+      int k0 = (xx & 15) * 256;
+      if (k0 < nkb) {
+        float* wd = (float*)(smem + 26880);
+        int NKP = (nkb + 63) & ~63;
+        int qpart = xx >> 4;
+        int qbeg = (qpart * nqb) >> 3;
+        int qend = ((qpart + 1) * nqb) >> 3;
+        int k = k0 + t;
+        const unsigned short* eb = eg + (size_t)b * EB_ELEM;
+        float acc = 0.f;
+        for (int qcv = qbeg; qcv < qend; qcv += 256) {
+          __syncthreads();
+          int qq = qcv + t;
+          float d = 0.f;
+          if (qq < qend) {
+            const float4* dp = (const float4*)(den_part + ((size_t)b * NN + qq) * NDEN);
+            float4 a0 = dp[0], a1 = dp[1], a2 = dp[2], a3 = dp[3];
+            d = ((a0.x + a0.y) + (a0.z + a0.w)) + ((a1.x + a1.y) + (a1.z + a1.w))
+              + ((a2.x + a2.y) + (a2.z + a2.w)) + ((a3.x + a3.y) + (a3.z + a3.w));
+          }
+          wd[t] = (d > 0.f) ? 1.f / d : 0.f;
+          __syncthreads();
+          int lim = min(256, qend - qcv);
+          if (k < nkb) {
+            const unsigned short* ep = eb + (size_t)qcv * NKP + k;
+            int j = 0;
+            for (; j + 8 <= lim; j += 8) {
+              #pragma unroll
+              for (int u = 0; u < 8; ++u)
+                acc += us2f(ep[(size_t)(j + u) * NKP]) * wd[j + u];
+            }
+            for (; j < lim; ++j)
+              acc += us2f(ep[(size_t)j * NKP]) * wd[j];
+          }
+        }
+        if (k < nkb) visp[((size_t)qpart * BB + b) * NN + k] = acc;
+      }
+    } else {
+      int q0 = (xx - 128) * 64;
+      if (q0 < nqb) {
+        unsigned short* pxa = (unsigned short*)smem;
+        unsigned short* f1s = (unsigned short*)(smem + 17408);
+        int* qpl = (int*)(smem + 26624);
+        int lane = t & 63;
+        int quad = lane >> 4, col = lane & 15;
+        int cb = (t >> 6) * 16;
+        const int* qix = qidx + b * NN;
+        const unsigned short* xtb = xt + (size_t)b * NN * 64;
+        const unsigned short* w1b = wall;
+        const unsigned short* w2b = wall + 8192;
+        const unsigned short* wfb = wall + 12288;
+        short8 a1[4], a2[2], af[4];
+        #pragma unroll
+        for (int kt = 0; kt < 4; ++kt) {
+          a1[kt] = *(const short8*)&w1b[(cb + col) * 128 + kt * 32 + quad * 8];
+          af[kt] = *(const short8*)&wfb[(cb + col) * 128 + kt * 32 + quad * 8];
+        }
+        #pragma unroll
+        for (int kt = 0; kt < 2; ++kt)
+          a2[kt] = *(const short8*)&w2b[(cb + col) * 64 + kt * 32 + quad * 8];
+        float b2v[4];
+        #pragma unroll
+        for (int r = 0; r < 4; ++r) b2v[r] = fb2[cb + quad * 4 + r];
+        if (t < 64) qpl[t] = (q0 + t < nqb) ? qix[q0 + t] : -1;
+        for (int idx = t; idx < 512; idx += 256) {
+          int q = idx >> 3, c8 = (idx & 7) * 8;
+          int qq = q0 + q;
+          uint4 pv = make_uint4(0u, 0u, 0u, 0u);
+          unsigned short pa8[8] = {0, 0, 0, 0, 0, 0, 0, 0};
+          if (qq < nqb) {
+            int qp = qix[qq];
+            pv = *(const uint4*)(xtb + (size_t)qp * 64 + c8);
+            const float* db = den_part + ((size_t)b * NN + qq) * NDEN;
+            float d = 0.f;
+            #pragma unroll
+            for (int p2 = 0; p2 < NDEN; ++p2) d += db[p2];
+            float av[8];
+            #pragma unroll
+            for (int j = 0; j < 8; ++j) av[j] = 0.f;
+            const unsigned short* ab = afc_part + ((size_t)b * NN + qq) * (NPARTS * 64) + c8;
+            #pragma unroll
+            for (int p2 = 0; p2 < NPARTS; ++p2) {
+              const uint4 u = *(const uint4*)(ab + p2 * 64);
+              const unsigned short* e8 = (const unsigned short*)&u;
+              #pragma unroll
+              for (int j = 0; j < 8; ++j) av[j] += us2f(e8[j]);
+            }
+            float invd = (d > 0.f) ? 1.f / d : 0.f;
+            #pragma unroll
+            for (int j = 0; j < 8; ++j) pa8[j] = f2bu(av[j] * invd);
+          }
+          *(uint4*)&pxa[q * FS + c8] = pv;
+          *(uint4*)&pxa[q * FS + 64 + c8] = *(const uint4*)&pa8[0];
+        }
+        __syncthreads();
+        #pragma unroll
+        for (int qt = 0; qt < 4; ++qt) {
+          f32x4 acc = {0.f, 0.f, 0.f, 0.f};
+          #pragma unroll
+          for (int kt = 0; kt < 4; ++kt) {
+            short8 bfrag = *(const short8*)&pxa[(qt * 16 + col) * FS + kt * 32 + quad * 8];
+            acc = __builtin_amdgcn_mfma_f32_16x16x32_bf16(a1[kt], bfrag, acc, 0, 0, 0);
+          }
+          #pragma unroll
+          for (int r = 0; r < 4; ++r)
+            f1s[(qt * 16 + col) * LS + cb + quad * 4 + r] = f2bu(acc[r]);
+        }
+        __syncthreads();
+        #pragma unroll
+        for (int qt = 0; qt < 4; ++qt) {
+          f32x4 acc = {0.f, 0.f, 0.f, 0.f};
+          #pragma unroll
+          for (int kt = 0; kt < 2; ++kt) {
+            short8 bfrag = *(const short8*)&f1s[(qt * 16 + col) * LS + kt * 32 + quad * 8];
+            acc = __builtin_amdgcn_mfma_f32_16x16x32_bf16(a2[kt], bfrag, acc, 0, 0, 0);
+          }
+          #pragma unroll
+          for (int r = 0; r < 4; ++r) {
+            float sg = 1.f / (1.f + __expf(-(acc[r] + b2v[r])));
+            int addr = (qt * 16 + col) * FS + 64 + cb + quad * 4 + r;
+            pxa[addr] = f2bu(us2f(pxa[addr]) * (1.f - sg));
+          }
+        }
+        __syncthreads();
+        #pragma unroll
+        for (int qt = 0; qt < 4; ++qt) {
+          f32x4 acc = {0.f, 0.f, 0.f, 0.f};
+          #pragma unroll
+          for (int kt = 0; kt < 4; ++kt) {
+            short8 bfrag = *(const short8*)&pxa[(qt * 16 + col) * FS + kt * 32 + quad * 8];
+            acc = __builtin_amdgcn_mfma_f32_16x16x32_bf16(af[kt], bfrag, acc, 0, 0, 0);
+          }
+          int qp = qpl[qt * 16 + col];
+          if (qp >= 0) {
+            #pragma unroll
+            for (int r = 0; r < 4; ++r)
+              outp[((size_t)b * CC + cb + quad * 4 + r) * NN + qp] = acc[r];
+          }
+        }
+      }
+    }
+  }
+  grid.sync();
+
+  for (int vb = blockIdx.x; vb < 64; vb += gridDim.x) {
+    int i = vb * 256 + t;
+    int b = i >> 12, k = i & 4095;
+    float v = 0.f;
+    if (k < nkv[b]) {
+      #pragma unroll
+      for (int p2 = 0; p2 < 8; ++p2) v += visp[((size_t)p2 * BB + b) * NN + k];
+      vis[b * NN + kidx[b * NN + k]] = v;
+    }
+    #pragma unroll
+    for (int off = 32; off > 0; off >>= 1) v = fmaxf(v, __shfl_down(v, off));
+    if ((t & 63) == 0) atomicMax(vmaxb, __float_as_uint(v));
+  }
+  grid.sync();
+
+  for (int vb = blockIdx.x; vb < 1024; vb += gridDim.x) {
+    int i4 = vb * 256 + t;
+    int b = i4 >> 16;
+    int rem = i4 & 65535;
+    int y = rem >> 7, x4 = (rem & 127) * 4;
+    float vm = __uint_as_float(vmaxb[0]);
+    if (!(vm > 0.f)) vm = 1.f;
+    float v = vis[b * NN + (y >> 3) * 64 + (x4 >> 3)] / vm;
+    ((float4*)out2)[i4] = make_float4(v, v, v, v);
+  }
 }
+
+extern "C" void kernel_launch(void* const* d_in, const int* in_sizes, int n_in,
+                              void* d_out, int out_size, void* d_ws, size_t ws_size,
+                              hipStream_t stream) {
+  const float* x    = (const float*)d_in[0];
+  const float* mask = (const float*)d_in[1];
+  const float* w1   = (const float*)d_in[2];
+  const float* w2c  = (const float*)d_in[3];
+  const float* fsw1 = (const float*)d_in[4];
+  const float* fsw2 = (const float*)d_in[5];
+  const float* fsb2 = (const float*)d_in[6];
+  const float* fswf = (const float*)d_in[7];
+  float* out = (float*)d_out;
+  char* wsb = (char*)d_ws;
+
+  int occ = 0;
+  hipOccupancyMaxActiveBlocksPerMultiprocessor(&occ, reinterpret_cast<const void*>(k_mega), 256, 0);
+  if (occ < 1) occ = 1;
+  int grid = occ * 256;
+  if (grid > 2048) grid = 2048;
+
+  void* args[] = {(void*)&x, (void*)&mask, (void*)&w1, (void*)&w2c,
+                  (void*)&fsw1, (void*)&fsw2, (void*)&fsb2, (void*)&fswf,
+                  (void*)&out, (void*)&wsb};
+  hipLaunchCooperativeKernel(reinterpret_cast<void*>(k_mega), dim3(grid), dim3(256),
+                             args, 0, stream);
+}
```

After: 386.9 us. +122.4%, slower.
